# Kernel optimization log

Measured on AMD Instinct MI355X. Metric: run time of the kernel, lower is better.

## Reference

```python
import jax, jax.numpy as jnp
import numpy as np

THETA = 10000.0


def apply_rope(x, positions, theta=THETA):
    # x: [B, H, N, D], positions: [1, N] or [B, N]
    D = x.shape[-1]
    inv_freq = 1.0 / (theta ** (jnp.arange(0, D, 2, dtype=jnp.float32) / D))  # [D/2]
    ang = positions.astype(jnp.float32)[:, None, :, None] * inv_freq  # [B_or_1, 1, N, D/2]
    cos, sin = jnp.cos(ang), jnp.sin(ang)
    x1 = x[..., 0::2]
    x2 = x[..., 1::2]
    r1 = x1 * cos - x2 * sin
    r2 = x1 * sin + x2 * cos
    # interleave back to [..., D]
    return jnp.stack([r1, r2], axis=-1).reshape(x.shape)


def setup_inputs() -> dict:
    key = jax.random.key(0)
    ks = jax.random.split(key, 5)
    B, N, d_model = 2, 2048, 1024
    s = 1.0 / np.sqrt(d_model)
    return {
        "x": jax.random.normal(ks[0], (B, N, d_model), dtype=jnp.float32),
        "Wq": jax.random.normal(ks[1], (d_model, d_model), dtype=jnp.float32) * s,
        "Wk": jax.random.normal(ks[2], (d_model, d_model), dtype=jnp.float32) * s,
        "Wv": jax.random.normal(ks[3], (d_model, d_model), dtype=jnp.float32) * s,
        "Wo": jax.random.normal(ks[4], (d_model, d_model), dtype=jnp.float32) * s,
        "token_positions": jnp.arange(N, dtype=jnp.int32)[None, :],
    }


def reference(x, Wq, Wk, Wv, Wo, token_positions):
    B, N, d_model = x.shape
    H = 16
    D = d_model // H
    # projections: out = x @ W.T  (einsum '... i, j i -> ... j')
    def proj(W):
        y = jnp.einsum('bni,ji->bnj', x, W)
        return y.reshape(B, N, H, D).transpose(0, 2, 1, 3)  # [B,H,N,D]
    q, k, v = proj(Wq), proj(Wk), proj(Wv)
    q = apply_rope(q, token_positions)
    k = apply_rope(k, token_positions)
    scale = 1.0 / jnp.sqrt(jnp.asarray(D, dtype=x.dtype))
    scores = jnp.einsum('bhid,bhjd->bhij', q, k) * scale  # [B,H,N,N]
    causal = jnp.tril(jnp.ones((N, N), dtype=bool))
    scores = jnp.where(causal[None, None], scores, -jnp.inf)
    w = jax.nn.softmax(scores, axis=-1)
    o = jnp.einsum('bhij,bhjd->bhid', w, v)  # [B,H,N,D]
    o = o.transpose(0, 2, 1, 3).reshape(B, N, d_model)
    return jnp.einsum('bni,ji->bnj', o, Wo)
```

## Files before the change

### kernel.cpp

```cpp
#include <hip/hip_runtime.h>

#define DMODEL 1024
#define NSEQ   2048
#define BSZ    2
#define NH     16
#define HD     64
#define MROWS  (BSZ*NSEQ)

using short8 = __attribute__((ext_vector_type(8))) short;
using f32x4  = __attribute__((ext_vector_type(4))) float;

__device__ __forceinline__ short f2b(float f) {
  unsigned u = __builtin_bit_cast(unsigned, f);
  u += 0x7fffu + ((u >> 16) & 1u);
  return (short)(u >> 16);
}

__device__ __forceinline__ void load_lds16(const void* g, void* l) {
  __builtin_amdgcn_global_load_lds((const __attribute__((address_space(1))) unsigned int*)g,
                                   (__attribute__((address_space(3))) unsigned int*)l,
                                   16, 0, 0);
}

__global__ void cvt_all(const float* __restrict__ x,  const float* __restrict__ Wq,
                        const float* __restrict__ Wk, const float* __restrict__ Wv,
                        const float* __restrict__ Wo, const int* __restrict__ pos,
                        short* __restrict__ xb,  short* __restrict__ wqb,
                        short* __restrict__ wkb, short* __restrict__ wvb,
                        short* __restrict__ wob, float* __restrict__ cs) {
  const int NX  = (BSZ * NSEQ * DMODEL) / 4;
  const int NW  = (DMODEL * DMODEL) / 4;
  const int NCV = NX + 4 * NW;
  const int TOT = NCV + NSEQ * 32;
  for (int i = blockIdx.x * blockDim.x + threadIdx.x; i < TOT; i += gridDim.x * blockDim.x) {
    if (i < NCV) {
      const float* src; short* dst; int off;
      if (i < NX) { src = x; dst = xb; off = i; }
      else {
        int j = i - NX; int s = j >> 18; off = j & (NW - 1);
        src = (s == 0) ? Wq : (s == 1) ? Wk : (s == 2) ? Wv : Wo;
        dst = (s == 0) ? wqb : (s == 1) ? wkb : (s == 2) ? wvb : wob;
      }
      float4 v = reinterpret_cast<const float4*>(src)[off];
      short4 r;
      r.x = f2b(v.x); r.y = f2b(v.y); r.z = f2b(v.z); r.w = f2b(v.w);
      reinterpret_cast<short4*>(dst)[off] = r;
    } else {
      int idx = i - NCV;
      int n = idx >> 5, p = idx & 31;
      float inv = powf(10000.0f, -(float)(2 * p) / 64.0f);
      float ang = (float)pos[n] * inv;
      cs[idx * 2]     = cosf(ang);
      cs[idx * 2 + 1] = sinf(ang);
    }
  }
}

__global__ __launch_bounds__(512, 1) void gemm_qkv3(
    const short* __restrict__ xb,
    const short* __restrict__ wq, const short* __restrict__ wk, const short* __restrict__ wv,
    const float* __restrict__ cs,
    short* __restrict__ qb, short* __restrict__ kb, short* __restrict__ vt) {
  __shared__ short Al[2][128 * 64];
  __shared__ short Bl[2][3][128 * 64];

  const int t   = threadIdx.x;
  const int l   = t & 63;
  const int wid = t >> 6;
  const int wr  = (wid >> 2) * 64;
  const int wc  = (wid & 3) * 32;

  const int id = blockIdx.x;
  const int bx = id & 31;
  const int np = id >> 5;
  const int arow0 = bx * 128;
  const int bcol0 = np * 128;

  const int tr = t >> 3;
  const int c8 = (t & 7) ^ ((t >> 3) & 7);
  const short* W3[3] = {wq, wk, wv};

  auto STAGE = [&](int kt, int buf) {
#pragma unroll
    for (int h = 0; h < 2; ++h)
      load_lds16(xb + (size_t)(arow0 + h * 64 + tr) * DMODEL + kt * 64 + c8 * 8,
                 &Al[buf][h * 4096 + wid * 512]);
#pragma unroll
    for (int p = 0; p < 3; ++p)
#pragma unroll
      for (int h = 0; h < 2; ++h)
        load_lds16(W3[p] + (size_t)(bcol0 + h * 64 + tr) * DMODEL + kt * 64 + c8 * 8,
                   &Bl[buf][p][h * 4096 + wid * 512]);
  };

  f32x4 acc[3][4][2];
#pragma unroll
  for (int p = 0; p < 3; ++p)
#pragma unroll
    for (int mi = 0; mi < 4; ++mi)
#pragma unroll
      for (int ni = 0; ni < 2; ++ni) acc[p][mi][ni] = f32x4{0.f, 0.f, 0.f, 0.f};

  const int lr  = l & 15;
  const int lcb = (l >> 4) << 4;

  STAGE(0, 0);
  int cur = 0;

  for (int kt = 0; kt < DMODEL / 64; ++kt) {
    if (kt + 1 < DMODEL / 64) {
      STAGE(kt + 1, cur ^ 1);
      asm volatile("s_waitcnt vmcnt(8)" ::: "memory");
    } else {
      asm volatile("s_waitcnt vmcnt(0)" ::: "memory");
    }
    asm volatile("s_barrier" ::: "memory");

    const char* Ab = reinterpret_cast<const char*>(&Al[cur][0]);
#pragma unroll
    for (int ks = 0; ks < 2; ++ks) {
      const int cb = ks * 64 + lcb;
      short8 af[4];
#pragma unroll
      for (int mi = 0; mi < 4; ++mi) {
        int r = wr + mi * 16 + lr;
        af[mi] = *reinterpret_cast<const short8*>(Ab + r * 128 + (cb ^ ((r & 7) << 4)));
      }
#pragma unroll
      for (int p = 0; p < 3; ++p) {
        const char* Bb = reinterpret_cast<const char*>(&Bl[cur][p][0]);
        short8 bf[2];
#pragma unroll
        for (int ni = 0; ni < 2; ++ni) {
          int r = wc + ni * 16 + lr;
          bf[ni] = *reinterpret_cast<const short8*>(Bb + r * 128 + (cb ^ ((r & 7) << 4)));
        }
#pragma unroll
        for (int mi = 0; mi < 4; ++mi)
#pragma unroll
          for (int ni = 0; ni < 2; ++ni)
            acc[p][mi][ni] = __builtin_amdgcn_mfma_f32_16x16x32_bf16(af[mi], bf[ni], acc[p][mi][ni], 0, 0, 0);
      }
    }
    asm volatile("s_barrier" ::: "memory");
    cur ^= 1;
  }

#pragma unroll
  for (int p = 0; p < 3; ++p) {
#pragma unroll
    for (int mi = 0; mi < 4; ++mi) {
#pragma unroll
      for (int ni = 0; ni < 2; ++ni) {
#pragma unroll
        for (int r = 0; r < 4; ++r) {
          float v = acc[p][mi][ni][r];
          int m = arow0 + wr + mi * 16 + ((l >> 4) << 2) + r;
          int j = bcol0 + wc + ni * 16 + (l & 15);
          int n = m & (NSEQ - 1);
          int b = m >> 11;
          int h = j >> 6, d = j & 63, pp = d >> 1;
          float pv = __shfl_xor(v, 1);
          if (p < 2) {
            float c = cs[(n * 32 + pp) * 2];
            float s = cs[(n * 32 + pp) * 2 + 1];
            float res = (d & 1) ? (pv * s + v * c) : (v * c - pv * s);
            if (p == 0) res *= 0.180336880f;
            short* dst = (p == 0) ? qb : kb;
            dst[(((size_t)(b * NH + h)) * NSEQ + n) * HD + d] = f2b(res);
          } else {
            vt[(((size_t)(b * NH + h)) * HD + d) * NSEQ + n] = f2b(v);
          }
        }
      }
    }
  }
}

__global__ __launch_bounds__(256, 2) void gemm_out(
    const short* __restrict__ ob, const short* __restrict__ wo, float* __restrict__ out) {
  __shared__ short As[3 * 64 * 64];
  __shared__ short Bs[3 * 128 * 64];
  const int t = threadIdx.x;
  const int l = t & 63;
  const int w4 = t >> 6;
  const int wrow = (w4 >> 1) * 32;
  const int wcol = (w4 & 1) * 64;
  const int id = blockIdx.x;
  const int arow0 = (id & 63) * 64;
  const int bcol0 = (id >> 6) * 128;

  const int tr = t >> 3;
  const int c8 = (t & 7) ^ (tr & 7);

  auto STAGE = [&](int kt, int buf) {
#pragma unroll
    for (int is = 0; is < 2; ++is)
      load_lds16(ob + (size_t)(arow0 + tr + is * 32) * DMODEL + kt * 64 + c8 * 8,
                 &As[buf * 4096 + is * 2048 + (t >> 6) * 512]);
#pragma unroll
    for (int is = 0; is < 4; ++is)
      load_lds16(wo + (size_t)(bcol0 + tr + is * 32) * DMODEL + kt * 64 + c8 * 8,
                 &Bs[buf * 8192 + is * 2048 + (t >> 6) * 512]);
  };

  f32x4 acc[2][4];
#pragma unroll
  for (int mi = 0; mi < 2; ++mi)
#pragma unroll
    for (int ni = 0; ni < 4; ++ni) acc[mi][ni] = f32x4{0.f, 0.f, 0.f, 0.f};

  const int lr  = l & 15;
  const int lcb = (l >> 4) << 4;
  const int irow = (l >> 4) << 2;

  STAGE(0, 0);
  int cur = 0;

  for (int kt = 0; kt < DMODEL / 64; ++kt) {
    const int nxt = (cur == 2) ? 0 : cur + 1;
    if (kt + 1 < DMODEL / 64) {
      STAGE(kt + 1, nxt);
      asm volatile("s_waitcnt vmcnt(6)" ::: "memory");
    } else {
      asm volatile("s_waitcnt vmcnt(0)" ::: "memory");
    }
    asm volatile("s_barrier" ::: "memory");

    const char* Ab = reinterpret_cast<const char*>(&As[cur * 4096]);
    const char* Bb = reinterpret_cast<const char*>(&Bs[cur * 8192]);
#pragma unroll
    for (int ks = 0; ks < 2; ++ks) {
      const int cb = ks * 64 + lcb;
      short8 af[2], bf[4];
#pragma unroll
      for (int mi = 0; mi < 2; ++mi) {
        int r = wrow + mi * 16 + lr;
        af[mi] = *reinterpret_cast<const short8*>(Ab + r * 128 + (cb ^ ((r & 7) << 4)));
      }
#pragma unroll
      for (int ni = 0; ni < 4; ++ni) {
        int r = wcol + ni * 16 + lr;
        bf[ni] = *reinterpret_cast<const short8*>(Bb + r * 128 + (cb ^ ((r & 7) << 4)));
      }
#pragma unroll
      for (int mi = 0; mi < 2; ++mi)
#pragma unroll
        for (int ni = 0; ni < 4; ++ni)
          acc[mi][ni] = __builtin_amdgcn_mfma_f32_16x16x32_bf16(af[mi], bf[ni], acc[mi][ni], 0, 0, 0);
    }
    cur = nxt;
  }

#pragma unroll
  for (int mi = 0; mi < 2; ++mi) {
#pragma unroll
    for (int ni = 0; ni < 4; ++ni) {
#pragma unroll
      for (int r = 0; r < 4; ++r) {
        int m = arow0 + wrow + mi * 16 + irow + r;
        int j = bcol0 + wcol + ni * 16 + (l & 15);
        out[(size_t)m * DMODEL + j] = acc[mi][ni][r];
      }
    }
  }
}

__global__ __launch_bounds__(1024, 1) void attn(
    const short* __restrict__ qb, const short* __restrict__ kb,
    const short* __restrict__ vt, short* __restrict__ ob) {
  __shared__ short Ks[3][128 * 64];
  __shared__ short Vs[3][64 * 128];
  __shared__ short Ps[16][16 * 64];
  const int t = threadIdx.x;
  const int l = t & 63;
  const int w = t >> 6;
  const int qs = w & 7;
  const int g  = w >> 3;
  const int id  = blockIdx.x;
  const int xcd = id & 7;
  const int bh  = xcd + 8 * (id >> 6);
  const int qy  = (id >> 3) & 7;
  const short* Q  = qb + (size_t)bh * NSEQ * HD;
  const short* Kg = kb + (size_t)bh * NSEQ * HD;
  const short* Vg = vt + (size_t)bh * HD * NSEQ;
  const int b = bh >> 4, h = bh & 15;

  const int trk = t >> 3;
  const int ck  = (t & 7) ^ ((t >> 3) & 7);
  const int trv = t >> 4;
  const int cv  = (t & 15) ^ ((t >> 4) & 15);
  const int irow = (l >> 4) << 2;
  const short8 ones = {(short)0x3F80, (short)0x3F80, (short)0x3F80, (short)0x3F80,
                       (short)0x3F80, (short)0x3F80, (short)0x3F80, (short)0x3F80};

  auto STAGEA = [&](int tile, int buf) {
    int j0 = tile * 128;
    load_lds16(Kg + (size_t)(j0 + trk) * HD + ck * 8, &Ks[buf][t * 8]);
    load_lds16(Vg + (size_t)trv * NSEQ + j0 + cv * 8, &Vs[buf][t * 8]);
  };

  int cur = 0;
  for (int pass = 0; pass < 2; ++pass) {
    const int qt = pass ? (15 - qy) : qy;
    const int q0 = qt * 128;
    const int nt = qt + 1;

    asm volatile("s_barrier" ::: "memory");
    STAGEA(0, cur);

    short8 qf[2];
    {
      int qrow = q0 + qs * 16 + (l & 15);
#pragma unroll
      for (int ks = 0; ks < 2; ++ks)
        qf[ks] = *reinterpret_cast<const short8*>(Q + (size_t)qrow * HD + ks * 32 + (l >> 4) * 8);
    }

    f32x4 ao[4];
#pragma unroll
    for (int dt = 0; dt < 4; ++dt) ao[dt] = f32x4{0.f, 0.f, 0.f, 0.f};
    f32x4 accl = f32x4{0.f, 0.f, 0.f, 0.f};

    for (int tile = 0; tile < nt; ++tile) {
      const int nxt = (cur == 2) ? 0 : cur + 1;
      if (tile + 1 < nt) {
        STAGEA(tile + 1, nxt);
        asm volatile("s_waitcnt vmcnt(2)" ::: "memory");
      } else {
        asm volatile("s_waitcnt vmcnt(0)" ::: "memory");
      }
      asm volatile("s_barrier" ::: "memory");

      const char* Kb = reinterpret_cast<const char*>(&Ks[cur][0]);
      const char* Vb = reinterpret_cast<const char*>(&Vs[cur][0]);

      f32x4 sc[4];
#pragma unroll
      for (int jt = 0; jt < 4; ++jt) sc[jt] = f32x4{0.f, 0.f, 0.f, 0.f};
#pragma unroll
      for (int ks = 0; ks < 2; ++ks) {
        const int cb = ks * 64 + ((l >> 4) * 16);
#pragma unroll
        for (int jt = 0; jt < 4; ++jt) {
          int kr = g * 64 + jt * 16 + (l & 15);
          short8 kf = *reinterpret_cast<const short8*>(Kb + kr * 128 + (cb ^ ((kr & 7) << 4)));
          sc[jt] = __builtin_amdgcn_mfma_f32_16x16x32_bf16(qf[ks], kf, sc[jt], 0, 0, 0);
        }
      }

      if (tile == nt - 1) {
        const int j0 = tile * 128 + g * 64;
#pragma unroll
        for (int jt = 0; jt < 4; ++jt)
#pragma unroll
          for (int r = 0; r < 4; ++r) {
            int i_g = q0 + qs * 16 + irow + r;
            int j_g = j0 + jt * 16 + (l & 15);
            if (j_g > i_g) sc[jt][r] = -1e30f;
          }
      }

#pragma unroll
      for (int jt = 0; jt < 4; ++jt) {
#pragma unroll
        for (int r = 0; r < 4; ++r) {
          float p = __builtin_amdgcn_exp2f(sc[jt][r]);
          int i = irow + r;
          int jj = jt * 16 + (l & 15);
          Ps[w][i * 64 + (jj ^ ((i & 7) << 3))] =
              (short)(__builtin_bit_cast(unsigned, p) >> 16);
        }
      }

#pragma unroll
      for (int ks2 = 0; ks2 < 2; ++ks2) {
        const int cb = ks2 * 64 + ((l >> 4) * 16);
        int pr = l & 15;
        short8 pf = *reinterpret_cast<const short8*>(
            reinterpret_cast<const char*>(&Ps[w][0]) + pr * 128 + (cb ^ ((pr & 7) << 4)));
        accl = __builtin_amdgcn_mfma_f32_16x16x32_bf16(pf, ones, accl, 0, 0, 0);
#pragma unroll
        for (int dt = 0; dt < 4; ++dt) {
          int vr = dt * 16 + (l & 15);
          short8 vf = *reinterpret_cast<const short8*>(
              Vb + vr * 256 + ((g * 128 + cb) ^ ((vr & 15) << 4)));
          ao[dt] = __builtin_amdgcn_mfma_f32_16x16x32_bf16(pf, vf, ao[dt], 0, 0, 0);
        }
      }
      cur = nxt;
    }
    asm volatile("s_barrier" ::: "memory");

    float* Opart = reinterpret_cast<float*>(&Ks[0][0]);
    float* Apart = reinterpret_cast<float*>(&Vs[0][0]);
    const int cswz = ((l >> 4) & 1) << 4;
    if (g == 1) {
#pragma unroll
      for (int dt = 0; dt < 4; ++dt)
#pragma unroll
        for (int r = 0; r < 4; ++r)
          Opart[qs * 1024 + (irow + r) * 64 + ((dt * 16 + (l & 15)) ^ cswz)] = ao[dt][r];
      if ((l & 15) == 0)
#pragma unroll
        for (int r = 0; r < 4; ++r)
          Apart[qs * 16 + irow + r] = accl[r];
    }
    asm volatile("s_barrier" ::: "memory");
    if (g == 0) {
#pragma unroll
      for (int dt = 0; dt < 4; ++dt)
#pragma unroll
        for (int r = 0; r < 4; ++r)
          ao[dt][r] += Opart[qs * 1024 + (irow + r) * 64 + ((dt * 16 + (l & 15)) ^ cswz)];
#pragma unroll
      for (int r = 0; r < 4; ++r)
        accl[r] += Apart[qs * 16 + irow + r];
#pragma unroll
      for (int dt = 0; dt < 4; ++dt)
#pragma unroll
        for (int r = 0; r < 4; ++r) {
          int n = q0 + qs * 16 + irow + r;
          int col = h * 64 + dt * 16 + (l & 15);
          ob[((size_t)b * NSEQ + n) * DMODEL + col] = f2b(ao[dt][r] / accl[r]);
        }
    }
  }
}

extern "C" void kernel_launch(void* const* d_in, const int* in_sizes, int n_in,
                              void* d_out, int out_size, void* d_ws, size_t ws_size,
                              hipStream_t stream) {
  const float* x  = (const float*)d_in[0];
  const float* Wq = (const float*)d_in[1];
  const float* Wk = (const float*)d_in[2];
  const float* Wv = (const float*)d_in[3];
  const float* Wo = (const float*)d_in[4];
  const int*   pos = (const int*)d_in[5];
  float* out = (float*)d_out;
  char* ws = (char*)d_ws;

  short* xb  = (short*)(ws);
  short* wqb = (short*)(ws + ((size_t)8  << 20));
  short* wkb = (short*)(ws + ((size_t)10 << 20));
  short* wvb = (short*)(ws + ((size_t)12 << 20));
  short* wob = (short*)(ws + ((size_t)14 << 20));
  short* qb  = (short*)(ws + ((size_t)16 << 20));
  short* kb  = (short*)(ws + ((size_t)24 << 20));
  short* vt  = (short*)(ws + ((size_t)32 << 20));
  short* ob  = (short*)(ws + ((size_t)40 << 20));
  float* cs  = (float*)(ws + ((size_t)48 << 20));

  cvt_all<<<2048, 256, 0, stream>>>(x, Wq, Wk, Wv, Wo, pos, xb, wqb, wkb, wvb, wob, cs);
  gemm_qkv3<<<256, 512, 0, stream>>>(xb, wqb, wkb, wvb, cs, qb, kb, vt);
  attn<<<256, 1024, 0, stream>>>(qb, kb, vt, ob);
  gemm_out<<<512, 256, 0, stream>>>(ob, wob, out);
}
```

Before: 92.71 us.

## Shrink QKV GEMM N-tile to 64, triple-buffer LDS, drop trailing barrier

The fused QKV projection now uses a 128x64 output tile per projection instead of 128x128, which doubles the grid from 256 to 512 blocks. This fills more of the 256 CUs and cuts the accumulator registers per wave. The LDS staging goes from double to triple buffering with a matching vmcnt wait, which makes it safe to remove the end-of-iteration barrier. In exchange, each block reloads the A tile for half as much output, so global and LDS traffic per FLOP rises.

Measured after the change: 104.1 us. 12.2% more time.

```diff
diff --git a/kernel.cpp b/kernel.cpp
--- a/kernel.cpp
+++ b/kernel.cpp
@@ -61,20 +61,20 @@
     const short* __restrict__ wq, const short* __restrict__ wk, const short* __restrict__ wv,
     const float* __restrict__ cs,
     short* __restrict__ qb, short* __restrict__ kb, short* __restrict__ vt) {
-  __shared__ short Al[2][128 * 64];
-  __shared__ short Bl[2][3][128 * 64];
+  __shared__ short Al[3][128 * 64];
+  __shared__ short Bl[3][3][64 * 64];
 
   const int t   = threadIdx.x;
   const int l   = t & 63;
   const int wid = t >> 6;
   const int wr  = (wid >> 2) * 64;
-  const int wc  = (wid & 3) * 32;
+  const int wc  = (wid & 3) * 16;
 
   const int id = blockIdx.x;
   const int bx = id & 31;
   const int np = id >> 5;
   const int arow0 = bx * 128;
-  const int bcol0 = np * 128;
+  const int bcol0 = np * 64;
 
   const int tr = t >> 3;
   const int c8 = (t & 7) ^ ((t >> 3) & 7);
@@ -87,19 +87,15 @@
                  &Al[buf][h * 4096 + wid * 512]);
 #pragma unroll
     for (int p = 0; p < 3; ++p)
-#pragma unroll
-      for (int h = 0; h < 2; ++h)
-        load_lds16(W3[p] + (size_t)(bcol0 + h * 64 + tr) * DMODEL + kt * 64 + c8 * 8,
-                   &Bl[buf][p][h * 4096 + wid * 512]);
+      load_lds16(W3[p] + (size_t)(bcol0 + tr) * DMODEL + kt * 64 + c8 * 8,
+                 &Bl[buf][p][wid * 512]);
   };
 
-  f32x4 acc[3][4][2];
+  f32x4 acc[3][4];
 #pragma unroll
   for (int p = 0; p < 3; ++p)
 #pragma unroll
-    for (int mi = 0; mi < 4; ++mi)
-#pragma unroll
-      for (int ni = 0; ni < 2; ++ni) acc[p][mi][ni] = f32x4{0.f, 0.f, 0.f, 0.f};
+    for (int mi = 0; mi < 4; ++mi) acc[p][mi] = f32x4{0.f, 0.f, 0.f, 0.f};
 
   const int lr  = l & 15;
   const int lcb = (l >> 4) << 4;
@@ -108,9 +104,10 @@
   int cur = 0;
 
   for (int kt = 0; kt < DMODEL / 64; ++kt) {
+    const int nxt = (cur == 2) ? 0 : cur + 1;
     if (kt + 1 < DMODEL / 64) {
-      STAGE(kt + 1, cur ^ 1);
-      asm volatile("s_waitcnt vmcnt(8)" ::: "memory");
+      STAGE(kt + 1, nxt);
+      asm volatile("s_waitcnt vmcnt(5)" ::: "memory");
     } else {
       asm volatile("s_waitcnt vmcnt(0)" ::: "memory");
     }
@@ -129,48 +126,39 @@
 #pragma unroll
       for (int p = 0; p < 3; ++p) {
         const char* Bb = reinterpret_cast<const char*>(&Bl[cur][p][0]);
-        short8 bf[2];
-#pragma unroll
-        for (int ni = 0; ni < 2; ++ni) {
-          int r = wc + ni * 16 + lr;
-          bf[ni] = *reinterpret_cast<const short8*>(Bb + r * 128 + (cb ^ ((r & 7) << 4)));
-        }
+        int r = wc + lr;
+        short8 bf = *reinterpret_cast<const short8*>(Bb + r * 128 + (cb ^ ((r & 7) << 4)));
 #pragma unroll
         for (int mi = 0; mi < 4; ++mi)
-#pragma unroll
-          for (int ni = 0; ni < 2; ++ni)
-            acc[p][mi][ni] = __builtin_amdgcn_mfma_f32_16x16x32_bf16(af[mi], bf[ni], acc[p][mi][ni], 0, 0, 0);
-      }
-    }
-    asm volatile("s_barrier" ::: "memory");
-    cur ^= 1;
-  }
-
+          acc[p][mi] = __builtin_amdgcn_mfma_f32_16x16x32_bf16(af[mi], bf, acc[p][mi], 0, 0, 0);
+      }
+    }
+    cur = nxt;
+  }
+
+  const int irow = (l >> 4) << 2;
 #pragma unroll
   for (int p = 0; p < 3; ++p) {
 #pragma unroll
     for (int mi = 0; mi < 4; ++mi) {
 #pragma unroll
-      for (int ni = 0; ni < 2; ++ni) {
-#pragma unroll
-        for (int r = 0; r < 4; ++r) {
-          float v = acc[p][mi][ni][r];
-          int m = arow0 + wr + mi * 16 + ((l >> 4) << 2) + r;
-          int j = bcol0 + wc + ni * 16 + (l & 15);
-          int n = m & (NSEQ - 1);
-          int b = m >> 11;
-          int h = j >> 6, d = j & 63, pp = d >> 1;
-          float pv = __shfl_xor(v, 1);
-          if (p < 2) {
-            float c = cs[(n * 32 + pp) * 2];
-            float s = cs[(n * 32 + pp) * 2 + 1];
-            float res = (d & 1) ? (pv * s + v * c) : (v * c - pv * s);
-            if (p == 0) res *= 0.180336880f;
-            short* dst = (p == 0) ? qb : kb;
-            dst[(((size_t)(b * NH + h)) * NSEQ + n) * HD + d] = f2b(res);
-          } else {
-            vt[(((size_t)(b * NH + h)) * HD + d) * NSEQ + n] = f2b(v);
-          }
+      for (int r = 0; r < 4; ++r) {
+        float v = acc[p][mi][r];
+        int m = arow0 + wr + mi * 16 + irow + r;
+        int j = bcol0 + wc + (l & 15);
+        int n = m & (NSEQ - 1);
+        int b = m >> 11;
+        int h = j >> 6, d = j & 63, pp = d >> 1;
+        float pv = __shfl_xor(v, 1);
+        if (p < 2) {
+          float c = cs[(n * 32 + pp) * 2];
+          float s = cs[(n * 32 + pp) * 2 + 1];
+          float res = (d & 1) ? (pv * s + v * c) : (v * c - pv * s);
+          if (p == 0) res *= 0.180336880f;
+          short* dst = (p == 0) ? qb : kb;
+          dst[(((size_t)(b * NH + h)) * NSEQ + n) * HD + d] = f2b(res);
+        } else {
+          vt[(((size_t)(b * NH + h)) * HD + d) * NSEQ + n] = f2b(v);
         }
       }
     }
@@ -452,7 +440,7 @@
   float* cs  = (float*)(ws + ((size_t)48 << 20));
 
   cvt_all<<<2048, 256, 0, stream>>>(x, Wq, Wk, Wv, Wo, pos, xb, wqb, wkb, wvb, wob, cs);
-  gemm_qkv3<<<256, 512, 0, stream>>>(xb, wqb, wkb, wvb, cs, qb, kb, vt);
+  gemm_qkv3<<<512, 512, 0, stream>>>(xb, wqb, wkb, wvb, cs, qb, kb, vt);
   attn<<<256, 1024, 0, stream>>>(qb, kb, vt, ob);
   gemm_out<<<512, 256, 0, stream>>>(ob, wob, out);
 }
```
